# Kernel tuning notes

Measured on AMD Instinct MI355X. Metric: run time of the kernel, lower is better.

The kernel has to match this reference:

```python
import jax, jax.numpy as jnp
import numpy as np

B, C, H, W, K = 16, 313, 128, 128, 5


def setup_inputs() -> dict:
    key = jax.random.key(0)
    k1, k2, k3, k4, k5, k6 = jax.random.split(key, 6)
    pred = jax.random.normal(k1, (B, C, H, W), dtype=jnp.float32)
    _color = jax.random.normal(k2, (B, 2, H, W), dtype=jnp.float32)
    binned_color = jax.random.randint(k3, (B, 1, H, W), 0, C, dtype=jnp.int64)
    knn_idx = jax.random.randint(k4, (C, K), 0, C, dtype=jnp.int64)
    knn_weights = jax.random.uniform(k5, (C, K), dtype=jnp.float32)
    # soft-encoding weights per bin normally sum to 1; normalize for realism
    knn_weights = knn_weights / jnp.sum(knn_weights, axis=1, keepdims=True)
    weights = jax.random.uniform(k6, (C,), dtype=jnp.float32)
    return {
        "pred": pred,
        "_color": _color,
        "binned_color": binned_color,
        "knn_idx": knn_idx,
        "knn_weights": knn_weights,
        "weights": weights,
    }


def reference(pred, _color, binned_color, knn_idx, knn_weights, weights):
    # log_softmax over the C bin channels: (B, C, H, W)
    logp = jax.nn.log_softmax(pred, axis=1)
    target_idx = binned_color[:, 0]                 # (B, H, W)
    idx = knn_idx[target_idx]                       # (B, H, W, K)
    wts = knn_weights[target_idx]                   # (B, H, W, K)
    w = weights[target_idx]                         # (B, H, W)
    idx_bkhw = jnp.transpose(idx, (0, 3, 1, 2))     # (B, K, H, W)
    wts_bkhw = jnp.transpose(wts, (0, 3, 1, 2))     # (B, K, H, W)
    p = jnp.take_along_axis(logp, idx_bkhw, axis=1)  # gather K bins per pixel
    loss = -jnp.mean(jnp.sum(p * wts_bkhw, axis=1) * w)
    return loss
```

## Files before the change

### kernel.cpp

```cpp
#include <hip/hip_runtime.h>


#define CC   313
#define HW   16384
#define NPIX 262144
#define KK   5

typedef float f4 __attribute__((ext_vector_type(4)));

__global__ __launch_bounds__(256, 4) void bcl_kernel(
    const float* __restrict__ pred,
    const int*   __restrict__ binned,
    const int*   __restrict__ knn_idx,
    const float* __restrict__ knn_w,
    const float* __restrict__ weights,
    float*       __restrict__ out)
{
    const int tid  = blockIdx.x * blockDim.x + threadIdx.x;
    const int lane = threadIdx.x & 63;
    const int wv   = tid >> 6;
    const int q    = lane >> 3;
    const int sub  = lane & 7;

    const int pb = wv * 32 + sub * 4;
    const int b  = pb >> 14;
    const int hw = pb & (HW - 1);

    const int4 t4 = *(const int4*)(binned + pb);
    const int t[4] = {t4.x, t4.y, t4.z, t4.w};

    int   ki[4][KK];
    float kw[4][KK];
    #pragma unroll
    for (int j = 0; j < 4; ++j) {
        #pragma unroll
        for (int k = 0; k < KK; ++k) {
            ki[j][k] = knn_idx[t[j] * KK + k];
            kw[j][k] = knn_w [t[j] * KK + k];
        }
    }

    const float* base = pred + (size_t)b * CC * HW + hw;

    float s[4]   = {0.f, 0.f, 0.f, 0.f};
    float dot[4] = {0.f, 0.f, 0.f, 0.f};

#define BODY(CIDX)                                                          \
    {                                                                       \
        const int cc = (CIDX);                                              \
        const f4 x = __builtin_nontemporal_load(                            \
                         (const f4*)(base + (size_t)cc * HW));              \
        const float xv[4] = {x.x, x.y, x.z, x.w};                           \
        _Pragma("unroll")                                                   \
        for (int j = 0; j < 4; ++j) {                                       \
            s[j] += __expf(xv[j]);                                          \
            float wsel = (cc == ki[j][0]) ? kw[j][0] :                      \
                         (cc == ki[j][1]) ? kw[j][1] :                      \
                         (cc == ki[j][2]) ? kw[j][2] :                      \
                         (cc == ki[j][3]) ? kw[j][3] :                      \
                         (cc == ki[j][4]) ? kw[j][4] : 0.0f;                \
            dot[j] = fmaf(xv[j], wsel, dot[j]);                             \
        }                                                                   \
    }

    int c = q;
    for (; c + 24 < CC; c += 32) {
        BODY(c);
        BODY(c + 8);
        BODY(c + 16);
        BODY(c + 24);
    }
    for (; c < CC; c += 8)
        BODY(c);
#undef BODY

    float tv = 0.0f;
    #pragma unroll
    for (int j = 0; j < 4; ++j) {
        float st = s[j], dt = dot[j];
        st += __shfl_xor(st, 8);  dt += __shfl_xor(dt, 8);
        st += __shfl_xor(st, 16); dt += __shfl_xor(dt, 16);
        st += __shfl_xor(st, 32); dt += __shfl_xor(dt, 32);
        if (q == 0) {
            const float sumw = kw[j][0] + kw[j][1] + kw[j][2] + kw[j][3] + kw[j][4];
            const float val  = dt - logf(st) * sumw;
            tv += val * weights[t[j]];
        }
    }

    #pragma unroll
    for (int off = 32; off > 0; off >>= 1)
        tv += __shfl_down(tv, off);

    __shared__ float red[4];
    if (lane == 0) red[threadIdx.x >> 6] = tv;
    __syncthreads();
    if (threadIdx.x == 0) {
        const float bs = red[0] + red[1] + red[2] + red[3];
        atomicAdd(out, bs * (-1.0f / (float)NPIX));
    }
}

extern "C" void kernel_launch(void* const* d_in, const int* in_sizes, int n_in,
                              void* d_out, int out_size, void* d_ws, size_t ws_size,
                              hipStream_t stream) {
    const float* pred    = (const float*)d_in[0];
    const int*   binned  = (const int*)  d_in[2];
    const int*   knn_idx = (const int*)  d_in[3];
    const float* knn_w   = (const float*)d_in[4];
    const float* weights = (const float*)d_in[5];
    float* out = (float*)d_out;

    hipMemsetAsync(out, 0, sizeof(float), stream);

    bcl_kernel<<<2048, 256, 0, stream>>>(pred, binned, knn_idx, knn_w, weights, out);
}
```

Before: 425.6 us.

## Assign each wave a contiguous pixel row and reduce channel partials via LDS

Remaps work so that each wave's 64 lanes load 1KB of one channel row contiguously, instead of eight 128B segments from different channels. The channel split moves from lanes within a wave to the 8 waves of a 512-thread block. Partial sums are combined through shared memory, with one atomic per block. The larger block and launch bounds can tighten the per-thread register budget and cause spills.

```diff
diff --git a/kernel.cpp b/kernel.cpp
--- a/kernel.cpp
+++ b/kernel.cpp
@@ -8,7 +8,7 @@
 
 typedef float f4 __attribute__((ext_vector_type(4)));
 
-__global__ __launch_bounds__(256, 4) void bcl_kernel(
+__global__ __launch_bounds__(512, 4) void bcl_kernel(
     const float* __restrict__ pred,
     const int*   __restrict__ binned,
     const int*   __restrict__ knn_idx,
@@ -16,13 +16,11 @@
     const float* __restrict__ weights,
     float*       __restrict__ out)
 {
-    const int tid  = blockIdx.x * blockDim.x + threadIdx.x;
     const int lane = threadIdx.x & 63;
-    const int wv   = tid >> 6;
-    const int q    = lane >> 3;
-    const int sub  = lane & 7;
+    const int r    = threadIdx.x >> 6;
+    const int grp  = blockIdx.x;
 
-    const int pb = wv * 32 + sub * 4;
+    const int pb = grp * 256 + lane * 4;
     const int b  = pb >> 14;
     const int hw = pb & (HW - 1);
 
@@ -47,7 +45,7 @@
 
 #define BODY(CIDX)                                                          \
     {                                                                       \
-        const int cc = (CIDX);                                              \
+        const int cc = (CIDX);           \
         const f4 x = __builtin_nontemporal_load(                            \
                          (const f4*)(base + (size_t)cc * HW));              \
         const float xv[4] = {x.x, x.y, x.z, x.w};                           \
@@ -63,7 +61,7 @@
         }                                                                   \
     }
 
-    int c = q;
+    int c = r;
     for (; c + 24 < CC; c += 32) {
         BODY(c);
         BODY(c + 8);
@@ -74,30 +72,33 @@
         BODY(c);
 #undef BODY
 
-    float tv = 0.0f;
+    __shared__ float ls[8][4][64];
+    __shared__ float ld[8][4][64];
     #pragma unroll
     for (int j = 0; j < 4; ++j) {
-        float st = s[j], dt = dot[j];
-        st += __shfl_xor(st, 8);  dt += __shfl_xor(dt, 8);
-        st += __shfl_xor(st, 16); dt += __shfl_xor(dt, 16);
-        st += __shfl_xor(st, 32); dt += __shfl_xor(dt, 32);
-        if (q == 0) {
+        ls[r][j][lane] = s[j];
+        ld[r][j][lane] = dot[j];
+    }
+    __syncthreads();
+
+    if (r == 0) {
+        float tv = 0.0f;
+        #pragma unroll
+        for (int j = 0; j < 4; ++j) {
+            float st = 0.f, dt = 0.f;
+            #pragma unroll
+            for (int w = 0; w < 8; ++w) {
+                st += ls[w][j][lane];
+                dt += ld[w][j][lane];
+            }
             const float sumw = kw[j][0] + kw[j][1] + kw[j][2] + kw[j][3] + kw[j][4];
-            const float val  = dt - logf(st) * sumw;
-            tv += val * weights[t[j]];
+            tv += (dt - logf(st) * sumw) * weights[t[j]];
         }
-    }
-
-    #pragma unroll
-    for (int off = 32; off > 0; off >>= 1)
-        tv += __shfl_down(tv, off);
-
-    __shared__ float red[4];
-    if (lane == 0) red[threadIdx.x >> 6] = tv;
-    __syncthreads();
-    if (threadIdx.x == 0) {
-        const float bs = red[0] + red[1] + red[2] + red[3];
-        atomicAdd(out, bs * (-1.0f / (float)NPIX));
+        #pragma unroll
+        for (int off = 32; off > 0; off >>= 1)
+            tv += __shfl_down(tv, off);
+        if (lane == 0)
+            atomicAdd(out, tv * (-1.0f / (float)NPIX));
     }
 }
 
@@ -113,5 +114,5 @@
 
     hipMemsetAsync(out, 0, sizeof(float), stream);
 
-    bcl_kernel<<<2048, 256, 0, stream>>>(pred, binned, knn_idx, knn_w, weights, out);
+    bcl_kernel<<<1024, 512, 0, stream>>>(pred, binned, knn_idx, knn_w, weights, out);
 }
```

After: 414.2 us. 2.7% less time.
